# Optimization experiments

Measured on AMD Instinct MI355X. Metric: run time of the kernel, lower is better.

The kernel has to match this reference:

```python
import jax, jax.numpy as jnp
import numpy as np

N = 100000       # nodes
E = 1600000      # edges (before self-loops)
IN = 32          # input_dim
HID = 64         # hidden_dim
HEADS = 4
HO = HID // HEADS  # per-head out of gat1
OUT = 32         # output_dim
HID2 = HID // 2
BN_EPS = 1e-5
NEG_SLOPE = 0.2  # PyG GATConv default leaky relu slope


def setup_inputs() -> dict:
    key = jax.random.key(0)
    ks = jax.random.split(key, 28)
    f32 = jnp.float32
    rn = lambda k, s, sc=0.1: jax.random.normal(k, s, f32) * sc
    inp = {}
    inp["x"] = jax.random.normal(ks[0], (N, IN), f32)
    inp["edge_index"] = jax.random.randint(ks[1], (2, E), 0, N, jnp.int32)
    # GATConv 1: in=IN, heads=HEADS, out/head=HO, concat
    inp["W1"] = rn(ks[2], (IN, HEADS * HO))
    inp["att_src1"] = rn(ks[3], (HEADS, HO))
    inp["att_dst1"] = rn(ks[4], (HEADS, HO))
    inp["b1"] = rn(ks[5], (HEADS * HO,))
    # GATConv 2: in=HID, heads=1, out=OUT, no concat (mean)
    inp["W2"] = rn(ks[6], (HID, OUT))
    inp["att_src2"] = rn(ks[7], (1, OUT))
    inp["att_dst2"] = rn(ks[8], (1, OUT))
    inp["b2"] = rn(ks[9], (OUT,))
    # BatchNorms (inference mode: running stats)
    inp["bn1_g"] = jnp.ones((HID,), f32)
    inp["bn1_b"] = jnp.zeros((HID,), f32)
    inp["bn1_m"] = rn(ks[10], (HID,), 0.1)
    inp["bn1_v"] = jax.random.uniform(ks[11], (HID,), f32, 0.5, 1.5)
    inp["bn2_g"] = jnp.ones((OUT,), f32)
    inp["bn2_b"] = jnp.zeros((OUT,), f32)
    inp["bn2_m"] = rn(ks[12], (OUT,), 0.1)
    inp["bn2_v"] = jax.random.uniform(ks[13], (OUT,), f32, 0.5, 1.5)
    # classifier: OUT -> HID2 -> 3
    inp["cls_w1"] = rn(ks[14], (OUT, HID2))
    inp["cls_b1"] = rn(ks[15], (HID2,))
    inp["cls_w2"] = rn(ks[16], (HID2, 3))
    inp["cls_b2"] = rn(ks[17], (3,))
    inp["reg_w1"] = rn(ks[18], (OUT, HID2))
    inp["reg_b1"] = rn(ks[19], (HID2,))
    inp["reg_w2"] = rn(ks[20], (HID2, 1))
    inp["reg_b2"] = rn(ks[21], (1,))
    return inp


def _segment_softmax(e, seg, n):
    # e: [E, H]; softmax over edges sharing the same destination segment
    m = jax.ops.segment_max(e, seg, num_segments=n)
    ex = jnp.exp(e - m[seg])
    s = jax.ops.segment_sum(ex, seg, num_segments=n)
    return ex / (s[seg] + 1e-16)


def _gat(x, src, dst, W, a_src, a_dst, b, heads, ho, concat):
    n = x.shape[0]
    h = (x @ W).reshape(n, heads, ho)                    # [N,H,F]
    e = (h * a_src).sum(-1)[src] + (h * a_dst).sum(-1)[dst]  # [E,H]
    e = jax.nn.leaky_relu(e, NEG_SLOPE)
    alpha = _segment_softmax(e, dst, n)                  # [E,H]
    out = jax.ops.segment_sum(h[src] * alpha[:, :, None], dst, num_segments=n)
    out = out.reshape(n, heads * ho) if concat else out.mean(axis=1)
    return out + b


def _bn(x, g, b, m, v):
    return (x - m) * jax.lax.rsqrt(v + BN_EPS) * g + b


def reference(x, edge_index, W1, att_src1, att_dst1, b1, W2, att_src2, att_dst2, b2,
              bn1_g, bn1_b, bn1_m, bn1_v, bn2_g, bn2_b, bn2_m, bn2_v,
              cls_w1, cls_b1, cls_w2, cls_b2, reg_w1, reg_b1, reg_w2, reg_b2):
    n = x.shape[0]
    # PyG GATConv default add_self_loops=True
    loops = jnp.arange(n, dtype=edge_index.dtype)
    src = jnp.concatenate([edge_index[0], loops])
    dst = jnp.concatenate([edge_index[1], loops])

    h = _gat(x, src, dst, W1, att_src1, att_dst1, b1, HEADS, HO, True)   # [N, HID]
    h = jax.nn.relu(_bn(h, bn1_g, bn1_b, bn1_m, bn1_v))
    emb = _gat(h, src, dst, W2, att_src2, att_dst2, b2, 1, OUT, False)   # [N, OUT]
    emb = jax.nn.relu(_bn(emb, bn2_g, bn2_b, bn2_m, bn2_v))

    roles = jax.nn.relu(emb @ cls_w1 + cls_b1) @ cls_w2 + cls_b2          # [N, 3]
    energy = jax.nn.relu(emb @ reg_w1 + reg_b1) @ reg_w2 + reg_b2         # [N, 1]
    return emb, roles, energy
```

## Files before the change

kernel.cpp:

```cpp
#include <hip/hip_runtime.h>
#include <hip/hip_bf16.h>

#define NN 100000
#define EE 1600000
#define ETOT (EE + NN)
#define IND 32
#define HIDD 64
#define NHEADS 4
#define OUTD 32
#define HID2D 32
#define LOG2E 1.44269504f

#define BSH 8
#define NBUCK 391
#define CAP 5120
#define EPB 8192
#define L2NB 128

typedef unsigned int uint;

__device__ __forceinline__ uint pack2(float a, float b) {
  uint lo = (uint)__bfloat16_as_ushort(__float2bfloat16(a));
  uint hi = (uint)__bfloat16_as_ushort(__float2bfloat16(b));
  return (hi << 16) | lo;
}
__device__ __forceinline__ float lo2f(uint w) { return __uint_as_float(w << 16); }
__device__ __forceinline__ float hi2r(uint w) { return __uint_as_float(w); }

__global__ __launch_bounds__(256) void k_lin1(
    const float* __restrict__ x, const float* __restrict__ W1,
    const float* __restrict__ atsrc, const float* __restrict__ atdst,
    uint* __restrict__ h1u, float* __restrict__ as1, float* __restrict__ ad1,
    int* __restrict__ bcur) {
  int t = threadIdx.x;
  if (blockIdx.x == 0) { bcur[t] = 0; bcur[t + 256] = 0; }
  int node = blockIdx.x * 256 + t;
  if (node >= NN) return;
  float e[IND];
  const float4* xr = (const float4*)(x + node * IND);
#pragma unroll
  for (int r = 0; r < IND / 4; r++) {
    float4 v = xr[r];
    e[4 * r] = v.x; e[4 * r + 1] = v.y; e[4 * r + 2] = v.z; e[4 * r + 3] = v.w;
  }
  uint* hrow = h1u + node * 32;
#pragma unroll 1
  for (int half = 0; half < 2; half++) {
    float a[32];
#pragma unroll
    for (int j = 0; j < 32; j++) a[j] = 0.f;
#pragma unroll 4
    for (int k = 0; k < IND; k++) {
      const float* wr = W1 + k * HIDD + half * 32;
      float ek = e[k];
#pragma unroll
      for (int j = 0; j < 32; j++) a[j] += ek * wr[j];
    }
#pragma unroll
    for (int q = 0; q < 16; q++) hrow[half * 16 + q] = pack2(a[2 * q], a[2 * q + 1]);
#pragma unroll
    for (int hh = 0; hh < 2; hh++) {
      int hd = half * 2 + hh;
      float ps = 0.f, pd = 0.f;
#pragma unroll
      for (int f = 0; f < 16; f++) {
        float av = a[hh * 16 + f];
        ps += av * atsrc[hd * 16 + f];
        pd += av * atdst[hd * 16 + f];
      }
      as1[node * NHEADS + hd] = ps * LOG2E;
      ad1[node * NHEADS + hd] = pd * LOG2E;
    }
  }
}

__global__ __launch_bounds__(256) void k_bin(const int* __restrict__ ei,
                                             int* __restrict__ bcur,
                                             int* __restrict__ bins) {
  __shared__ int cnt[NBUCK];
  int t = threadIdx.x;
  for (int i = t; i < NBUCK; i += 256) cnt[i] = 0;
  __syncthreads();
  int base = blockIdx.x * EPB;
  int lim = base + EPB; if (lim > ETOT) lim = ETOT;
  for (int i = base + t; i < lim; i += 256) {
    int d = (i < EE) ? ei[EE + i] : (i - EE);
    atomicAdd(&cnt[d >> BSH], 1);
  }
  __syncthreads();
  for (int i = t; i < NBUCK; i += 256) cnt[i] = atomicAdd(&bcur[i], cnt[i]);
  __syncthreads();
  for (int i = base + t; i < lim; i += 256) {
    int s, d;
    if (i < EE) { s = ei[i]; d = ei[EE + i]; } else { s = i - EE; d = s; }
    int bk = d >> BSH;
    int pos = atomicAdd(&cnt[bk], 1);
    bins[bk * CAP + pos] = (s << BSH) | (d & ((1 << BSH) - 1));
  }
}

__global__ __launch_bounds__(256) void k_csr(const int* __restrict__ bcur,
                                             const int* __restrict__ bins,
                                             int* __restrict__ rowp,
                                             int* __restrict__ srcs) {
  __shared__ int lrec[CAP];
  __shared__ int sA[512], sB[512];
  __shared__ int ldeg[256];
  int b = blockIdx.x, t = threadIdx.x;
  if (b == 0 && t == 0) rowp[NN] = ETOT;
  sA[t] = (t < NBUCK) ? bcur[t] : 0;
  sA[t + 256] = (t + 256 < NBUCK) ? bcur[t + 256] : 0;
  __syncthreads();
  int* in = sA; int* out = sB;
  for (int off = 1; off < 512; off <<= 1) {
    for (int i = t; i < 512; i += 256)
      out[i] = in[i] + ((i >= off) ? in[i - off] : 0);
    __syncthreads();
    int* tmp = in; in = out; out = tmp;
  }
  int gb = (b == 0) ? 0 : in[b - 1];
  __syncthreads();
  int count = bcur[b]; if (count > CAP) count = CAP;
  ldeg[t] = 0;
  __syncthreads();
  for (int i = t; i < count; i += 256) {
    int r = bins[b * CAP + i];
    lrec[i] = r;
    atomicAdd(&ldeg[r & 255], 1);
  }
  __syncthreads();
  int dv = ldeg[t];
  sA[t] = dv;
  __syncthreads();
  in = sA; out = sB;
  for (int off = 1; off < 256; off <<= 1) {
    out[t] = in[t] + ((t >= off) ? in[t - off] : 0);
    __syncthreads();
    int* tmp = in; in = out; out = tmp;
  }
  int nb = b << BSH;
  int ex = in[t] - dv;
  if (nb + t < NN) rowp[nb + t] = gb + ex;
  ldeg[t] = ex;
  __syncthreads();
  for (int i = t; i < count; i += 256) {
    int r = lrec[i];
    int pos = atomicAdd(&ldeg[r & 255], 1);
    srcs[gb + pos] = (r >> BSH) << 3;
  }
}

__global__ __launch_bounds__(256, 4) void k_agg1(
    const int* __restrict__ rowp, const int* __restrict__ srcs,
    const uint* __restrict__ h1u, const float* __restrict__ as1,
    const float* __restrict__ ad1, const float* __restrict__ b1,
    const float* __restrict__ g, const float* __restrict__ bb,
    const float* __restrict__ m, const float* __restrict__ v,
    float* __restrict__ hbn) {
  int t = threadIdx.x;
  int wid = t >> 6, lane = t & 63;
  int n0 = blockIdx.x * 16 + wid * 4;
  int slot = lane >> 3;
  int fl = lane & 7;
  int hd = fl >> 1;
  int rp[5];
#pragma unroll
  for (int k = 0; k < 5; k++) rp[k] = rowp[n0 + k];
  const uint4* h14 = (const uint4*)h1u;
  float acc[4][8], l[4], adv[4], as[4];
  int p[4], p1[4], lp[4], en[4], s1v[4];
  uint4 w[4];
#pragma unroll
  for (int k = 0; k < 4; k++) {
    adv[k] = ad1[(n0 + k) * NHEADS + hd];
    en[k] = rp[k + 1];
    lp[k] = en[k] - 1;
    p[k] = rp[k] + slot;
    int pc = p[k] < lp[k] ? p[k] : lp[k];
    int s0 = srcs[pc];
    w[k] = h14[s0 + fl];
    as[k] = as1[(s0 >> 1) + hd];
    p1[k] = p[k] + 8;
    int pc1 = p1[k] < lp[k] ? p1[k] : lp[k];
    s1v[k] = srcs[pc1];
    l[k] = 0.f;
#pragma unroll
    for (int i = 0; i < 8; i++) acc[k][i] = 0.f;
  }
  while (p[0] < en[0] || p[1] < en[1] || p[2] < en[2] || p[3] < en[3]) {
    uint4 wn[4]; float an[4]; int s2[4];
#pragma unroll
    for (int k = 0; k < 4; k++) {
      wn[k] = h14[s1v[k] + fl];
      an[k] = as1[(s1v[k] >> 1) + hd];
      int p2 = p1[k] + 8;
      int pc = p2 < lp[k] ? p2 : lp[k];
      s2[k] = srcs[pc];
    }
#pragma unroll
    for (int k = 0; k < 4; k++) {
      if (p[k] < en[k]) {
        float e = as[k] + adv[k];
        e = fmaxf(e, 0.2f * e);
        float ex = exp2f(e);
        l[k] += ex;
        acc[k][0] += ex * lo2f(w[k].x); acc[k][1] += ex * hi2r(w[k].x);
        acc[k][2] += ex * lo2f(w[k].y); acc[k][3] += ex * hi2r(w[k].y);
        acc[k][4] += ex * lo2f(w[k].z); acc[k][5] += ex * hi2r(w[k].z);
        acc[k][6] += ex * lo2f(w[k].w); acc[k][7] += ex * hi2r(w[k].w);
      }
      w[k] = wn[k]; as[k] = an[k]; s1v[k] = s2[k];
      p[k] = p1[k]; p1[k] += 8;
    }
  }
#pragma unroll
  for (int off = 8; off <= 32; off <<= 1) {
#pragma unroll
    for (int k = 0; k < 4; k++) {
#pragma unroll
      for (int i = 0; i < 8; i++) acc[k][i] += __shfl_xor(acc[k][i], off, 64);
      l[k] += __shfl_xor(l[k], off, 64);
    }
  }
  if (slot < 4) {
    float lsum = 0.f, av[8];
#pragma unroll
    for (int i = 0; i < 8; i++) av[i] = 0.f;
#pragma unroll
    for (int k = 0; k < 4; k++) {
      if (slot == k) {
        lsum = l[k];
#pragma unroll
        for (int i = 0; i < 8; i++) av[i] = acc[k][i];
      }
    }
    int node = n0 + slot;
    float li = 1.f / (lsum + 1e-16f);
    int fb = fl * 8;
    float o[8];
#pragma unroll
    for (int i = 0; i < 8; i++) {
      int j = fb + i;
      float ov = av[i] * li + b1[j];
      ov = (ov - m[j]) * rsqrtf(v[j] + 1e-5f) * g[j] + bb[j];
      o[i] = fmaxf(ov, 0.f);
    }
    float4* dst = (float4*)(hbn + node * HIDD + fb);
    dst[0] = make_float4(o[0], o[1], o[2], o[3]);
    dst[1] = make_float4(o[4], o[5], o[6], o[7]);
  }
}

__global__ __launch_bounds__(256) void k_lin2(
    const float* __restrict__ hbn, const float* __restrict__ W2,
    const float* __restrict__ atsrc, const float* __restrict__ atdst,
    uint* __restrict__ h2u, float* __restrict__ as2, float* __restrict__ ad2) {
  __shared__ float xsT[HIDD][L2NB];
  __shared__ float Wp[HIDD * OUTD];
  __shared__ float atS[OUTD], atD[OUTD];
  int t = threadIdx.x;
  int nb = blockIdx.x * L2NB;
  for (int i = t; i < HIDD * OUTD; i += 256) Wp[i] = W2[i];
  if (t < OUTD) { atS[t] = atsrc[t]; atD[t] = atdst[t]; }
#pragma unroll
  for (int i = 0; i < 8; i++) {
    int idx = t + i * 256;
    int node = idx >> 4, c = idx & 15;
    int gnode = nb + node;
    float4 vv = make_float4(0.f, 0.f, 0.f, 0.f);
    if (gnode < NN) vv = ((const float4*)hbn)[gnode * 16 + c];
    int ns = node ^ ((c & 7) << 2);
    xsT[4 * c + 0][ns] = vv.x;
    xsT[4 * c + 1][ns] = vv.y;
    xsT[4 * c + 2][ns] = vv.z;
    xsT[4 * c + 3][ns] = vv.w;
  }
  __syncthreads();
  int w = t >> 6, lane = t & 63;
  int gq = lane >> 3, tl = lane & 7;
  int base = w * 32 + gq * 4;
  int j0 = tl * 4;
  float acc[4][4];
#pragma unroll
  for (int e = 0; e < 4; e++)
#pragma unroll
    for (int d = 0; d < 4; d++) acc[e][d] = 0.f;
#pragma unroll 4
  for (int k = 0; k < HIDD; k++) {
    float4 wv = *(const float4*)&Wp[k * OUTD + j0];
    int swz = ((k >> 2) & 7) << 2;
    float4 xv = *(const float4*)&xsT[k][base ^ swz];
    acc[0][0] += xv.x * wv.x; acc[0][1] += xv.x * wv.y;
    acc[0][2] += xv.x * wv.z; acc[0][3] += xv.x * wv.w;
    acc[1][0] += xv.y * wv.x; acc[1][1] += xv.y * wv.y;
    acc[1][2] += xv.y * wv.z; acc[1][3] += xv.y * wv.w;
    acc[2][0] += xv.z * wv.x; acc[2][1] += xv.z * wv.y;
    acc[2][2] += xv.z * wv.z; acc[2][3] += xv.z * wv.w;
    acc[3][0] += xv.w * wv.x; acc[3][1] += xv.w * wv.y;
    acc[3][2] += xv.w * wv.z; acc[3][3] += xv.w * wv.w;
  }
#pragma unroll
  for (int e = 0; e < 4; e++) {
    int node = nb + base + e;
    float ps = acc[e][0] * atS[j0] + acc[e][1] * atS[j0 + 1] +
               acc[e][2] * atS[j0 + 2] + acc[e][3] * atS[j0 + 3];
    float pd = acc[e][0] * atD[j0] + acc[e][1] * atD[j0 + 1] +
               acc[e][2] * atD[j0 + 2] + acc[e][3] * atD[j0 + 3];
#pragma unroll
    for (int off = 1; off <= 4; off <<= 1) {
      ps += __shfl_xor(ps, off, 64);
      pd += __shfl_xor(pd, off, 64);
    }
    if (node < NN) {
      uint2 pk;
      pk.x = pack2(acc[e][0], acc[e][1]);
      pk.y = pack2(acc[e][2], acc[e][3]);
      ((uint2*)h2u)[node * 8 + tl] = pk;
      if (tl == 0) { as2[node] = ps * LOG2E; ad2[node] = pd * LOG2E; }
    }
  }
}

__global__ __launch_bounds__(256, 4) void k_agg2(
    const int* __restrict__ rowp, const int* __restrict__ srcs,
    const uint* __restrict__ h2u, const float* __restrict__ as2,
    const float* __restrict__ ad2, const float* __restrict__ b2v,
    const float* __restrict__ g, const float* __restrict__ bb,
    const float* __restrict__ m, const float* __restrict__ v,
    float* __restrict__ out_emb) {
  int t = threadIdx.x;
  int wid = t >> 6, lane = t & 63;
  int n0 = blockIdx.x * 16 + wid * 4;
  int slot = lane >> 3;
  int fl = lane & 7;
  int rp[5];
#pragma unroll
  for (int k = 0; k < 5; k++) rp[k] = rowp[n0 + k];
  const uint2* h22 = (const uint2*)h2u;
  float acc[4][4], l[4], adv[4], as[4];
  int p[4], p1[4], lp[4], en[4], s1v[4];
  uint2 w[4];
#pragma unroll
  for (int k = 0; k < 4; k++) {
    adv[k] = ad2[n0 + k];
    en[k] = rp[k + 1];
    lp[k] = en[k] - 1;
    p[k] = rp[k] + slot;
    int pc = p[k] < lp[k] ? p[k] : lp[k];
    int s0 = srcs[pc];
    w[k] = h22[s0 + fl];
    as[k] = as2[s0 >> 3];
    p1[k] = p[k] + 8;
    int pc1 = p1[k] < lp[k] ? p1[k] : lp[k];
    s1v[k] = srcs[pc1];
    l[k] = 0.f;
#pragma unroll
    for (int i = 0; i < 4; i++) acc[k][i] = 0.f;
  }
  while (p[0] < en[0] || p[1] < en[1] || p[2] < en[2] || p[3] < en[3]) {
    uint2 wn[4]; float an[4]; int s2[4];
#pragma unroll
    for (int k = 0; k < 4; k++) {
      wn[k] = h22[s1v[k] + fl];
      an[k] = as2[s1v[k] >> 3];
      int p2 = p1[k] + 8;
      int pc = p2 < lp[k] ? p2 : lp[k];
      s2[k] = srcs[pc];
    }
#pragma unroll
    for (int k = 0; k < 4; k++) {
      if (p[k] < en[k]) {
        float e = as[k] + adv[k];
        e = fmaxf(e, 0.2f * e);
        float ex = exp2f(e);
        l[k] += ex;
        acc[k][0] += ex * lo2f(w[k].x); acc[k][1] += ex * hi2r(w[k].x);
        acc[k][2] += ex * lo2f(w[k].y); acc[k][3] += ex * hi2r(w[k].y);
      }
      w[k] = wn[k]; as[k] = an[k]; s1v[k] = s2[k];
      p[k] = p1[k]; p1[k] += 8;
    }
  }
#pragma unroll
  for (int off = 8; off <= 32; off <<= 1) {
#pragma unroll
    for (int k = 0; k < 4; k++) {
#pragma unroll
      for (int i = 0; i < 4; i++) acc[k][i] += __shfl_xor(acc[k][i], off, 64);
      l[k] += __shfl_xor(l[k], off, 64);
    }
  }
  if (slot < 4) {
    float lsum = 0.f, av[4];
#pragma unroll
    for (int i = 0; i < 4; i++) av[i] = 0.f;
#pragma unroll
    for (int k = 0; k < 4; k++) {
      if (slot == k) {
        lsum = l[k];
#pragma unroll
        for (int i = 0; i < 4; i++) av[i] = acc[k][i];
      }
    }
    int node = n0 + slot;
    float li = 1.f / (lsum + 1e-16f);
    int fb = fl * 4;
    float o[4];
#pragma unroll
    for (int i = 0; i < 4; i++) {
      int j = fb + i;
      float ov = av[i] * li + b2v[j];
      ov = (ov - m[j]) * rsqrtf(v[j] + 1e-5f) * g[j] + bb[j];
      o[i] = fmaxf(ov, 0.f);
    }
    *(float4*)(out_emb + node * OUTD + fb) = make_float4(o[0], o[1], o[2], o[3]);
  }
}

__global__ __launch_bounds__(256) void k_mlp(
    const float* __restrict__ embf,
    const float* __restrict__ cw1, const float* __restrict__ cb1,
    const float* __restrict__ cw2, const float* __restrict__ cb2,
    const float* __restrict__ rw1, const float* __restrict__ rb1,
    const float* __restrict__ rw2, const float* __restrict__ rb2,
    float* __restrict__ out_roles, float* __restrict__ out_energy) {
  int node = blockIdx.x * 256 + threadIdx.x;
  if (node >= NN) return;
  float e[OUTD];
  const float4* er = (const float4*)(embf + node * OUTD);
#pragma unroll
  for (int r = 0; r < OUTD / 4; r++) {
    float4 v = er[r];
    e[4 * r] = v.x; e[4 * r + 1] = v.y; e[4 * r + 2] = v.z; e[4 * r + 3] = v.w;
  }
  float h[HID2D];
#pragma unroll
  for (int j = 0; j < HID2D; j++) h[j] = cb1[j];
#pragma unroll 4
  for (int k = 0; k < OUTD; k++) {
    const float* wr = cw1 + k * HID2D;
    float ek = e[k];
#pragma unroll
    for (int j = 0; j < HID2D; j++) h[j] += ek * wr[j];
  }
  float r0 = cb2[0], r1 = cb2[1], r2 = cb2[2];
#pragma unroll
  for (int j = 0; j < HID2D; j++) {
    float hv = fmaxf(h[j], 0.f);
    r0 += hv * cw2[j * 3 + 0];
    r1 += hv * cw2[j * 3 + 1];
    r2 += hv * cw2[j * 3 + 2];
  }
  out_roles[node * 3 + 0] = r0;
  out_roles[node * 3 + 1] = r1;
  out_roles[node * 3 + 2] = r2;
#pragma unroll
  for (int j = 0; j < HID2D; j++) h[j] = rb1[j];
#pragma unroll 4
  for (int k = 0; k < OUTD; k++) {
    const float* wr = rw1 + k * HID2D;
    float ek = e[k];
#pragma unroll
    for (int j = 0; j < HID2D; j++) h[j] += ek * wr[j];
  }
  float en = rb2[0];
#pragma unroll
  for (int j = 0; j < HID2D; j++) en += fmaxf(h[j], 0.f) * rw2[j];
  out_energy[node] = en;
}

extern "C" void kernel_launch(void* const* d_in, const int* in_sizes, int n_in,
                              void* d_out, int out_size, void* d_ws, size_t ws_size,
                              hipStream_t stream) {
  const float* x    = (const float*)d_in[0];
  const int*   ei   = (const int*)d_in[1];
  const float* W1   = (const float*)d_in[2];
  const float* as1w = (const float*)d_in[3];
  const float* ad1w = (const float*)d_in[4];
  const float* b1   = (const float*)d_in[5];
  const float* W2   = (const float*)d_in[6];
  const float* as2w = (const float*)d_in[7];
  const float* ad2w = (const float*)d_in[8];
  const float* b2v  = (const float*)d_in[9];
  const float* bn1g = (const float*)d_in[10];
  const float* bn1b = (const float*)d_in[11];
  const float* bn1m = (const float*)d_in[12];
  const float* bn1v = (const float*)d_in[13];
  const float* bn2g = (const float*)d_in[14];
  const float* bn2b = (const float*)d_in[15];
  const float* bn2m = (const float*)d_in[16];
  const float* bn2v = (const float*)d_in[17];
  const float* cw1  = (const float*)d_in[18];
  const float* cb1  = (const float*)d_in[19];
  const float* cw2  = (const float*)d_in[20];
  const float* cb2  = (const float*)d_in[21];
  const float* rw1  = (const float*)d_in[22];
  const float* rb1  = (const float*)d_in[23];
  const float* rw2  = (const float*)d_in[24];
  const float* rb2  = (const float*)d_in[25];

  uint*  h1u = (uint*)d_ws;
  float* hbn = (float*)(h1u + NN * 32);
  float* as1 = hbn + NN * HIDD;
  float* ad1 = as1 + NN * NHEADS;
  int* rowp  = (int*)(ad1 + NN * NHEADS);
  int* srcs  = rowp + NN + 1;
  int* bcur  = srcs + ETOT;
  int* bins  = bcur + 512;
  uint* h2u  = h1u;
  float* as2 = as1;
  float* ad2 = ad1;

  float* out        = (float*)d_out;
  float* out_emb    = out;
  float* out_roles  = out + NN * OUTD;
  float* out_energy = out + NN * (OUTD + 3);

  k_lin1<<<NBUCK, 256, 0, stream>>>(x, W1, as1w, ad1w, h1u, as1, ad1, bcur);
  k_bin<<<(ETOT + EPB - 1) / EPB, 256, 0, stream>>>(ei, bcur, bins);
  k_csr<<<NBUCK, 256, 0, stream>>>(bcur, bins, rowp, srcs);
  k_agg1<<<NN / 16, 256, 0, stream>>>(rowp, srcs, h1u, as1, ad1, b1, bn1g, bn1b, bn1m, bn1v, hbn);
  k_lin2<<<(NN + L2NB - 1) / L2NB, 256, 0, stream>>>(hbn, W2, as2w, ad2w, h2u, as2, ad2);
  k_agg2<<<NN / 16, 256, 0, stream>>>(rowp, srcs, h2u, as2, ad2, b2v, bn2g, bn2b, bn2m, bn2v, out_emb);
  k_mlp<<<(NN + 255) / 256, 256, 0, stream>>>(out_emb, cw1, cb1, cw2, cb2, rw1, rb1, rw2, rb2, out_roles, out_energy);
}
```

Baseline: 293.6 us.

## Replace shared-memory tiled layer-2 linear with one-thread-per-node register GEMV

The layer-2 projection kernel drops the transposed, swizzled shared-memory tile and 4x4 register blocking. Each thread now owns one node: it loads the 64-wide row into registers and computes 32 outputs in two halves of 16, reading W2 and the attention vectors straight from global memory as uniform loads. This removes the LDS staging, the barrier and the shuffle reductions. In exchange each thread does uncoalesced strided row loads and needs many registers, and the launch grid is reused from the bucket count, which happens to equal ceil(N/256).

```diff
diff --git a/kernel.cpp b/kernel.cpp
--- a/kernel.cpp
+++ b/kernel.cpp
@@ -15,7 +15,6 @@
 #define NBUCK 391
 #define CAP 5120
 #define EPB 8192
-#define L2NB 128
 
 typedef unsigned int uint;
 
@@ -255,70 +254,39 @@
     const float* __restrict__ hbn, const float* __restrict__ W2,
     const float* __restrict__ atsrc, const float* __restrict__ atdst,
     uint* __restrict__ h2u, float* __restrict__ as2, float* __restrict__ ad2) {
-  __shared__ float xsT[HIDD][L2NB];
-  __shared__ float Wp[HIDD * OUTD];
-  __shared__ float atS[OUTD], atD[OUTD];
-  int t = threadIdx.x;
-  int nb = blockIdx.x * L2NB;
-  for (int i = t; i < HIDD * OUTD; i += 256) Wp[i] = W2[i];
-  if (t < OUTD) { atS[t] = atsrc[t]; atD[t] = atdst[t]; }
-#pragma unroll
-  for (int i = 0; i < 8; i++) {
-    int idx = t + i * 256;
-    int node = idx >> 4, c = idx & 15;
-    int gnode = nb + node;
-    float4 vv = make_float4(0.f, 0.f, 0.f, 0.f);
-    if (gnode < NN) vv = ((const float4*)hbn)[gnode * 16 + c];
-    int ns = node ^ ((c & 7) << 2);
-    xsT[4 * c + 0][ns] = vv.x;
-    xsT[4 * c + 1][ns] = vv.y;
-    xsT[4 * c + 2][ns] = vv.z;
-    xsT[4 * c + 3][ns] = vv.w;
-  }
-  __syncthreads();
-  int w = t >> 6, lane = t & 63;
-  int gq = lane >> 3, tl = lane & 7;
-  int base = w * 32 + gq * 4;
-  int j0 = tl * 4;
-  float acc[4][4];
-#pragma unroll
-  for (int e = 0; e < 4; e++)
-#pragma unroll
-    for (int d = 0; d < 4; d++) acc[e][d] = 0.f;
-#pragma unroll 4
-  for (int k = 0; k < HIDD; k++) {
-    float4 wv = *(const float4*)&Wp[k * OUTD + j0];
-    int swz = ((k >> 2) & 7) << 2;
-    float4 xv = *(const float4*)&xsT[k][base ^ swz];
-    acc[0][0] += xv.x * wv.x; acc[0][1] += xv.x * wv.y;
-    acc[0][2] += xv.x * wv.z; acc[0][3] += xv.x * wv.w;
-    acc[1][0] += xv.y * wv.x; acc[1][1] += xv.y * wv.y;
-    acc[1][2] += xv.y * wv.z; acc[1][3] += xv.y * wv.w;
-    acc[2][0] += xv.z * wv.x; acc[2][1] += xv.z * wv.y;
-    acc[2][2] += xv.z * wv.z; acc[2][3] += xv.z * wv.w;
-    acc[3][0] += xv.w * wv.x; acc[3][1] += xv.w * wv.y;
-    acc[3][2] += xv.w * wv.z; acc[3][3] += xv.w * wv.w;
-  }
-#pragma unroll
-  for (int e = 0; e < 4; e++) {
-    int node = nb + base + e;
-    float ps = acc[e][0] * atS[j0] + acc[e][1] * atS[j0 + 1] +
-               acc[e][2] * atS[j0 + 2] + acc[e][3] * atS[j0 + 3];
-    float pd = acc[e][0] * atD[j0] + acc[e][1] * atD[j0 + 1] +
-               acc[e][2] * atD[j0 + 2] + acc[e][3] * atD[j0 + 3];
-#pragma unroll
-    for (int off = 1; off <= 4; off <<= 1) {
-      ps += __shfl_xor(ps, off, 64);
-      pd += __shfl_xor(pd, off, 64);
-    }
-    if (node < NN) {
-      uint2 pk;
-      pk.x = pack2(acc[e][0], acc[e][1]);
-      pk.y = pack2(acc[e][2], acc[e][3]);
-      ((uint2*)h2u)[node * 8 + tl] = pk;
-      if (tl == 0) { as2[node] = ps * LOG2E; ad2[node] = pd * LOG2E; }
-    }
-  }
+  int node = blockIdx.x * 256 + threadIdx.x;
+  if (node >= NN) return;
+  float e[HIDD];
+  const float4* xr = (const float4*)(hbn + node * HIDD);
+#pragma unroll
+  for (int r = 0; r < HIDD / 4; r++) {
+    float4 v = xr[r];
+    e[4 * r] = v.x; e[4 * r + 1] = v.y; e[4 * r + 2] = v.z; e[4 * r + 3] = v.w;
+  }
+  uint* hrow = h2u + node * 16;
+  float ps = 0.f, pd = 0.f;
+#pragma unroll 1
+  for (int half = 0; half < 2; half++) {
+    float a[16];
+#pragma unroll
+    for (int j = 0; j < 16; j++) a[j] = 0.f;
+#pragma unroll
+    for (int k = 0; k < HIDD; k++) {
+      const float* wr = W2 + k * OUTD + half * 16;
+      float ek = e[k];
+#pragma unroll
+      for (int j = 0; j < 16; j++) a[j] += ek * wr[j];
+    }
+#pragma unroll
+    for (int q = 0; q < 8; q++) hrow[half * 8 + q] = pack2(a[2 * q], a[2 * q + 1]);
+#pragma unroll
+    for (int j = 0; j < 16; j++) {
+      ps += a[j] * atsrc[half * 16 + j];
+      pd += a[j] * atdst[half * 16 + j];
+    }
+  }
+  as2[node] = ps * LOG2E;
+  ad2[node] = pd * LOG2E;
 }
 
 __global__ __launch_bounds__(256, 4) void k_agg2(
@@ -520,7 +488,7 @@
   k_bin<<<(ETOT + EPB - 1) / EPB, 256, 0, stream>>>(ei, bcur, bins);
   k_csr<<<NBUCK, 256, 0, stream>>>(bcur, bins, rowp, srcs);
   k_agg1<<<NN / 16, 256, 0, stream>>>(rowp, srcs, h1u, as1, ad1, b1, bn1g, bn1b, bn1m, bn1v, hbn);
-  k_lin2<<<(NN + L2NB - 1) / L2NB, 256, 0, stream>>>(hbn, W2, as2w, ad2w, h2u, as2, ad2);
+  k_lin2<<<NBUCK, 256, 0, stream>>>(hbn, W2, as2w, ad2w, h2u, as2, ad2);
   k_agg2<<<NN / 16, 256, 0, stream>>>(rowp, srcs, h2u, as2, ad2, b2v, bn2g, bn2b, bn2m, bn2v, out_emb);
   k_mlp<<<(NN + 255) / 256, 256, 0, stream>>>(out_emb, cw1, cb1, cw2, cb2, rw1, rb1, rw2, rb2, out_roles, out_energy);
 }
```

New measurement: 299.2 us. About the same (+1.9%).
